# Performance work log

Measured on AMD Instinct MI355X. Metric: run time of the kernel, lower is better.

## Reference

```python
import jax, jax.numpy as jnp
import numpy as np

EMPTY = -1  # sentinel for empty (vertex, region) slots, as in the TF layer


def setup_inputs() -> dict:
    key = jax.random.key(0)
    m, vertices, regions = 128, 2048, 32
    # values in [-1, vertices): -1 marks an empty slot, otherwise a vertex id
    mapping = jax.random.randint(key, (m, vertices, regions), EMPTY, vertices, dtype=jnp.int32)
    return {"mapping": mapping}


def reference(mapping):
    """Faithful JAX version of Graph2Col.call.

    TF's tf.where(mask) emits coordinates of True entries in row-major order
    with a data-dependent row count. For jit-compatibility we emit a
    fixed-size [m*V*R, ...] result where valid entries come first (same
    row-major order as tf.where) and padding rows are filled with -1.
    """
    m, V, R = mapping.shape
    total = m * V * R
    flat_map = mapping.reshape(-1)                 # [total]
    # row index is never -1, so the reduce_all mask is simply mapping != -1
    flat_mask = flat_map != EMPTY                  # [total] bool

    # stable stream compaction: valid entries first, preserving row-major order
    order = jnp.argsort(~flat_mask)                # stable sort -> tf.where ordering
    valid = flat_mask[order]                       # [total] bool

    rows = order // (V * R)
    rem = order % (V * R)
    verts = rem // R
    regs = rem % R

    # column_indices: coordinates of non-empty slots (tf.where returns int64)
    column_indices = jnp.stack([rows, verts, regs], axis=-1).astype(jnp.int64)  # [total, 3]
    # nodes_indices: (batch_row, vertex_id) gathered at those coordinates (int32)
    nodes_indices = jnp.stack([rows.astype(jnp.int32), flat_map[order]], axis=-1)  # [total, 2]

    column_indices = jnp.where(valid[:, None], column_indices, jnp.int64(EMPTY))
    nodes_indices = jnp.where(valid[:, None], nodes_indices, jnp.int32(EMPTY))
    return nodes_indices, column_indices
```

## Files before the change

### kernel.cpp

```cpp
#include <hip/hip_runtime.h>


#define EMPTY_V (-1)

typedef int v4i __attribute__((ext_vector_type(4)));

constexpr int TOTAL = 8388608;
constexpr int BLOCK = 256;
constexpr int CHUNK = 2048;
constexpr int NB = TOTAL / CHUNK;
constexpr int SUBT = CHUNK / (BLOCK * 4);
constexpr int NWAVE = BLOCK / 64;

__global__ __launch_bounds__(BLOCK) void k_count(const int* __restrict__ in,
                                                 int* __restrict__ counts) {
    const int b = blockIdx.x;
    const int tid = threadIdx.x;
    const int4* p = (const int4*)(in + (size_t)b * CHUNK);
    int c = 0;
#pragma unroll
    for (int s = 0; s < SUBT; ++s) {
        int4 v = p[s * BLOCK + tid];
        c += (v.x != EMPTY_V) + (v.y != EMPTY_V) + (v.z != EMPTY_V) + (v.w != EMPTY_V);
    }
    for (int d = 32; d; d >>= 1) c += __shfl_down(c, d, 64);
    __shared__ int ws[NWAVE];
    const int lane = tid & 63, wid = tid >> 6;
    if (lane == 0) ws[wid] = c;
    __syncthreads();
    if (tid == 0) counts[b] = ws[0] + ws[1] + ws[2] + ws[3];
}

__device__ __forceinline__ void copy_out(int* __restrict__ dst,
                                         const int* __restrict__ src,
                                         int ndw, int tid) {
    const int mis = (int)(((uintptr_t)dst >> 2) & 3);
    int peel = mis ? (4 - mis) : 0;
    if (peel > ndw) peel = ndw;
    if (tid < peel) dst[tid] = src[tid];
    const int body = (ndw - peel) >> 2;
    v4i* d4 = (v4i*)(dst + peel);
    const int* s4 = src + peel;
    for (int k = tid; k < body; k += BLOCK) {
        v4i t = {s4[4 * k], s4[4 * k + 1], s4[4 * k + 2], s4[4 * k + 3]};
        d4[k] = t;
    }
    const int tails = ndw - peel - 4 * body;
    if (tid < tails) {
        const int ld = peel + 4 * body + tid;
        dst[ld] = src[ld];
    }
}

__global__ __launch_bounds__(BLOCK) void k_scatter(const int* __restrict__ in,
                                                   const int* __restrict__ counts,
                                                   int* __restrict__ out_nodes,
                                                   int* __restrict__ out_cols) {
    const int b = blockIdx.x;
    const int tid = threadIdx.x;
    const int lane = tid & 63, wid = tid >> 6;
    const unsigned long long below = lane ? ((~0ull) >> (64 - lane)) : 0ull;

    __shared__ int s_nodes[2 * CHUNK];
    __shared__ int s_cols[3 * CHUNK];
    int* RED = s_nodes;
    int* WSUM = s_nodes + NWAVE;

    {
        int pa = 0;
        const int idx0 = tid * 16;
#pragma unroll
        for (int q = 0; q < 4; ++q) {
            const int4 c4 = ((const int4*)counts)[4 * tid + q];
            const int cs[4] = {c4.x, c4.y, c4.z, c4.w};
#pragma unroll
            for (int j = 0; j < 4; ++j)
                if (idx0 + 4 * q + j < b) pa += cs[j];
        }
        for (int d = 32; d; d >>= 1) pa += __shfl_down(pa, d, 64);
        if (lane == 0) RED[wid] = pa;
    }

    int4 v[SUBT];
    int pre[SUBT];
    const int4* p = (const int4*)(in + (size_t)b * CHUNK);
#pragma unroll
    for (int s = 0; s < SUBT; ++s) {
        v[s] = p[s * BLOCK + tid];
        const unsigned long long b0 = __ballot(v[s].x != EMPTY_V);
        const unsigned long long b1 = __ballot(v[s].y != EMPTY_V);
        const unsigned long long b2 = __ballot(v[s].z != EMPTY_V);
        const unsigned long long b3 = __ballot(v[s].w != EMPTY_V);
        pre[s] = __popcll(b0 & below) + __popcll(b1 & below) +
                 __popcll(b2 & below) + __popcll(b3 & below);
        if (lane == 0)
            WSUM[s * NWAVE + wid] =
                __popcll(b0) + __popcll(b1) + __popcll(b2) + __popcll(b3);
    }
    __syncthreads();

    const int excl = RED[0] + RED[1] + RED[2] + RED[3];
    int myoff[SUBT];
    int acc = 0;
#pragma unroll
    for (int s = 0; s < SUBT; ++s) {
        int cs_ = 0, woff = 0;
#pragma unroll
        for (int w = 0; w < NWAVE; ++w) {
            const int x = WSUM[s * NWAVE + w];
            cs_ += x;
            if (w < wid) woff += x;
        }
        myoff[s] = acc + woff + pre[s];
        acc += cs_;
    }
    const int blockValid = acc;
    __syncthreads();

    const int row = b >> 5;
#pragma unroll
    for (int s = 0; s < SUBT; ++s) {
        int lp = myoff[s];
        const int rem0 = ((b & 31) << 11) + (s << 10) + (tid << 2);
        const int vals[4] = {v[s].x, v[s].y, v[s].z, v[s].w};
#pragma unroll
        for (int j = 0; j < 4; ++j) {
            if (vals[j] != EMPTY_V) {
                const int pp = rem0 + j;
                s_nodes[2 * lp] = row;
                s_nodes[2 * lp + 1] = vals[j];
                s_cols[3 * lp] = row;
                s_cols[3 * lp + 1] = pp >> 5;
                s_cols[3 * lp + 2] = pp & 31;
                ++lp;
            }
        }
    }
    __syncthreads();

    copy_out(out_nodes + 2 * (size_t)excl, s_nodes, 2 * blockValid, tid);
    copy_out(out_cols + 3 * (size_t)excl, s_cols, 3 * blockValid, tid);

    {
        const int inv_pref = b * CHUNK - excl;
        const int start = TOTAL - inv_pref - (CHUNK - blockValid);
        const int end = TOTAL - inv_pref;
        for (int pos = start + tid; pos < end; pos += BLOCK) {
            out_nodes[2 * pos]     = EMPTY_V;
            out_nodes[2 * pos + 1] = EMPTY_V;
            out_cols[3 * pos]      = EMPTY_V;
            out_cols[3 * pos + 1]  = EMPTY_V;
            out_cols[3 * pos + 2]  = EMPTY_V;
        }
    }
}

extern "C" void kernel_launch(void* const* d_in, const int* in_sizes, int n_in,
                              void* d_out, int out_size, void* d_ws, size_t ws_size,
                              hipStream_t stream) {
    const int* in = (const int*)d_in[0];
    int* out = (int*)d_out;
    int* out_nodes = out;
    int* out_cols = out + 2 * (size_t)TOTAL;
    int* counts = (int*)d_ws;

    k_count<<<NB, BLOCK, 0, stream>>>(in, counts);
    k_scatter<<<NB, BLOCK, 0, stream>>>(in, counts, out_nodes, out_cols);
}
```

Measured before the change: 189.4 us.

## Fuse count and scatter into single-pass decoupled look-back scan kernel

Replaces the separate count kernel and per-block prefix recomputation with one kernel. It uses a dynamic block ticket and a decoupled look-back over per-block status flags to get each block's exclusive offset. This removes a second full read of the 32 MB input and one kernel launch. In exchange it adds a memset of the status array, serialized look-back latency, and spin-waits on global atomics.

After: 610.1 us. 222% more time.

```diff
diff --git a/kernel.cpp b/kernel.cpp
--- a/kernel.cpp
+++ b/kernel.cpp
@@ -12,24 +12,6 @@
 constexpr int SUBT = CHUNK / (BLOCK * 4);
 constexpr int NWAVE = BLOCK / 64;
 
-__global__ __launch_bounds__(BLOCK) void k_count(const int* __restrict__ in,
-                                                 int* __restrict__ counts) {
-    const int b = blockIdx.x;
-    const int tid = threadIdx.x;
-    const int4* p = (const int4*)(in + (size_t)b * CHUNK);
-    int c = 0;
-#pragma unroll
-    for (int s = 0; s < SUBT; ++s) {
-        int4 v = p[s * BLOCK + tid];
-        c += (v.x != EMPTY_V) + (v.y != EMPTY_V) + (v.z != EMPTY_V) + (v.w != EMPTY_V);
-    }
-    for (int d = 32; d; d >>= 1) c += __shfl_down(c, d, 64);
-    __shared__ int ws[NWAVE];
-    const int lane = tid & 63, wid = tid >> 6;
-    if (lane == 0) ws[wid] = c;
-    __syncthreads();
-    if (tid == 0) counts[b] = ws[0] + ws[1] + ws[2] + ws[3];
-}
 
 __device__ __forceinline__ void copy_out(int* __restrict__ dst,
                                          const int* __restrict__ src,
@@ -52,34 +34,22 @@
     }
 }
 
-__global__ __launch_bounds__(BLOCK) void k_scatter(const int* __restrict__ in,
-                                                   const int* __restrict__ counts,
-                                                   int* __restrict__ out_nodes,
-                                                   int* __restrict__ out_cols) {
-    const int b = blockIdx.x;
+__global__ __launch_bounds__(BLOCK) void k_fused(const int* __restrict__ in,
+                                                 int* __restrict__ ticket,
+                                                 unsigned* __restrict__ status,
+                                                 int* __restrict__ out_nodes,
+                                                 int* __restrict__ out_cols) {
     const int tid = threadIdx.x;
     const int lane = tid & 63, wid = tid >> 6;
     const unsigned long long below = lane ? ((~0ull) >> (64 - lane)) : 0ull;
 
     __shared__ int s_nodes[2 * CHUNK];
     __shared__ int s_cols[3 * CHUNK];
-    int* RED = s_nodes;
-    int* WSUM = s_nodes + NWAVE;
+    int* WSUM = s_nodes + 0;
 
-    {
-        int pa = 0;
-        const int idx0 = tid * 16;
-#pragma unroll
-        for (int q = 0; q < 4; ++q) {
-            const int4 c4 = ((const int4*)counts)[4 * tid + q];
-            const int cs[4] = {c4.x, c4.y, c4.z, c4.w};
-#pragma unroll
-            for (int j = 0; j < 4; ++j)
-                if (idx0 + 4 * q + j < b) pa += cs[j];
-        }
-        for (int d = 32; d; d >>= 1) pa += __shfl_down(pa, d, 64);
-        if (lane == 0) RED[wid] = pa;
-    }
+    if (tid == 0) s_nodes[12] = atomicAdd(ticket, 1);
+    __syncthreads();
+    const int b = s_nodes[12];
 
     int4 v[SUBT];
     int pre[SUBT];
@@ -99,7 +69,6 @@
     }
     __syncthreads();
 
-    const int excl = RED[0] + RED[1] + RED[2] + RED[3];
     int myoff[SUBT];
     int acc = 0;
 #pragma unroll
@@ -115,6 +84,55 @@
         acc += cs_;
     }
     const int blockValid = acc;
+
+    if (wid == 0) {
+        if (b == 0) {
+            if (lane == 0) {
+                __hip_atomic_store(&status[0], 0x20000000u | (unsigned)blockValid,
+                                   __ATOMIC_RELEASE, __HIP_MEMORY_SCOPE_AGENT);
+                s_nodes[13] = 0;
+            }
+        } else {
+            if (lane == 0)
+                __hip_atomic_store(&status[b], 0x10000000u | (unsigned)blockValid,
+                                   __ATOMIC_RELEASE, __HIP_MEMORY_SCOPE_AGENT);
+            int excl = 0, idx = b;
+            while (true) {
+                const int pb = idx - 1 - lane;
+                unsigned st;
+                if (pb >= 0) {
+                    do {
+                        st = __hip_atomic_load(&status[pb], __ATOMIC_ACQUIRE,
+                                               __HIP_MEMORY_SCOPE_AGENT);
+                    } while ((st >> 28) == 0u);
+                } else {
+                    st = 0x20000000u;
+                }
+                const unsigned fl = st >> 28;
+                int contrib = (int)(st & 0x0FFFFFFFu);
+                const unsigned long long pm = __ballot(fl == 2u);
+                if (pm) {
+                    const int Lmin = __ffsll((unsigned long long)pm) - 1;
+                    if (lane > Lmin) contrib = 0;
+                    for (int d = 32; d; d >>= 1) contrib += __shfl_down(contrib, d, 64);
+                    excl += contrib;
+                    break;
+                } else {
+                    for (int d = 32; d; d >>= 1) contrib += __shfl_down(contrib, d, 64);
+                    excl += contrib;
+                    idx -= 64;
+                }
+            }
+            if (lane == 0) {
+                __hip_atomic_store(&status[b],
+                                   0x20000000u | (unsigned)(excl + blockValid),
+                                   __ATOMIC_RELEASE, __HIP_MEMORY_SCOPE_AGENT);
+                s_nodes[13] = excl;
+            }
+        }
+    }
+    __syncthreads();
+    const int excl = s_nodes[13];
     __syncthreads();
 
     const int row = b >> 5;
@@ -162,8 +180,9 @@
     int* out = (int*)d_out;
     int* out_nodes = out;
     int* out_cols = out + 2 * (size_t)TOTAL;
-    int* counts = (int*)d_ws;
+    int* ticket = (int*)d_ws;
+    unsigned* status = (unsigned*)d_ws + 1;
 
-    k_count<<<NB, BLOCK, 0, stream>>>(in, counts);
-    k_scatter<<<NB, BLOCK, 0, stream>>>(in, counts, out_nodes, out_cols);
+    hipMemsetAsync(d_ws, 0, (NB + 1) * sizeof(int), stream);
+    k_fused<<<NB, BLOCK, 0, stream>>>(in, ticket, status, out_nodes, out_cols);
 }
```
